# Performance work log

Hardware: AMD Instinct MI355X
Metric: run time of the kernel (lower is better)

The kernel has to match this reference:

```python
import jax, jax.numpy as jnp
import numpy as np

N_E = 1024
E_DIM = 256
BETA = 0.25


def setup_inputs() -> dict:
    key = jax.random.key(0)
    k1, k2 = jax.random.split(key)
    z = jax.random.normal(k1, (16, E_DIM, 64, 64), dtype=jnp.float32)
    # nn.Embedding weight init: uniform(-1/n_e, 1/n_e)
    embedding = jax.random.uniform(
        k2, (N_E, E_DIM), dtype=jnp.float32, minval=-1.0 / N_E, maxval=1.0 / N_E
    )
    return {"z": z, "embedding": embedding}


def reference(z, embedding):
    n_e, e_dim = embedding.shape
    # 'b c ... -> b ... c'
    zt = jnp.moveaxis(z, 1, -1)  # [B, H, W, C]
    zf = zt.reshape(-1, e_dim)   # [N, C]
    # squared distances ||zf||^2 + ||e||^2 - 2 zf e^T  -> [N, n_e]
    d = (
        jnp.sum(zf * zf, axis=1, keepdims=True)
        + jnp.sum(embedding * embedding, axis=1)
        - 2.0 * (zf @ embedding.T)
    )
    idx = jnp.argmin(d, axis=1)  # [N] int32
    # direct embedding gather (equivalent to one-hot @ embedding)
    z_q = embedding[idx].reshape(zt.shape)  # [B, H, W, C]
    # commitment / codebook loss (reduction='mean')
    loss = jnp.mean((jax.lax.stop_gradient(z_q) - zt) ** 2) + BETA * jnp.mean(
        (z_q - jax.lax.stop_gradient(zt)) ** 2
    )
    # straight-through estimator
    z_q_st = zt + jax.lax.stop_gradient(z_q - zt)
    # perplexity from code usage histogram (equals mean of one-hot rows)
    counts = jnp.zeros((n_e,), dtype=jnp.float32).at[idx].add(1.0)
    e_mean = counts / zf.shape[0]
    perplexity = jnp.exp(-jnp.sum(e_mean * jnp.log(e_mean + 1e-10)))
    # 'b ... c -> b c ...'
    z_q_out = jnp.moveaxis(z_q_st, -1, 1)  # [B, C, H, W]
    return z_q_out, loss, perplexity, idx
```

## Files before the change

### kernel.cpp

```cpp
#include <hip/hip_runtime.h>

typedef _Float16 half8 __attribute__((ext_vector_type(8)));
typedef float f32x16 __attribute__((ext_vector_type(16)));

#define EDIM 256
#define NE   1024
#define HW   4096

#define ZQ_OFF   0
#define LOSS_OFF 16777216
#define PERP_OFF 16777217
#define IDX_OFF  16777218

#define WS_ESPH    0
#define WS_BNORM   (1024*1024)
#define WS_COUNTS  (WS_BNORM + 4096)
#define WS_COUNTER (WS_COUNTS + 4096)
#define WS_LOSS    (WS_COUNTER + 16)
#define WS_AN      (WS_LOSS + 16)
#define WS_IDX     (WS_AN + 65536*4)
#define WS_LIST    (WS_IDX + 65536*4)
#define WS_ET      (WS_LIST + 65536*4)

#define EPS 3.0e-4f
#define GEPS (512.0f * EPS)

#define AS1 __attribute__((address_space(1)))
#define AS3 __attribute__((address_space(3)))

__device__ __forceinline__ float np_half128(const float* __restrict__ p, long stride) {
#pragma clang fp contract(off)
    float r[8];
#pragma unroll
    for (int j = 0; j < 8; ++j) { float v = p[(long)j * stride]; r[j] = v * v; }
    for (int i = 8; i < 128; i += 8) {
#pragma unroll
        for (int j = 0; j < 8; ++j) { float v = p[(long)(i + j) * stride]; r[j] += v * v; }
    }
    return ((r[0] + r[1]) + (r[2] + r[3])) + ((r[4] + r[5]) + (r[6] + r[7]));
}

__global__ void k_prep_e(const float* __restrict__ e, _Float16* __restrict__ eh) {
    int t = blockIdx.x * 256 + threadIdx.x;
    int j = t >> 8, c = t & 255;
    float v = e[t] * 1024.0f;
    _Float16 h = (_Float16)v;
    int jt = j >> 7, nt = (j >> 5) & 3, lm = j & 31;
    int kc = c >> 5, r = c & 31, kh = r >> 4, hb = (r >> 3) & 1, kk = r & 7;
    int chunk = (((jt * 8 + kc) * 4 + nt) * 2 + kh) * 64 + hb * 32 + lm;
    eh[chunk * 8 + kk] = h;
}

__global__ void k_transpose(const float* __restrict__ e, float* __restrict__ eT) {
    __shared__ float tile[32][257];
    int b = blockIdx.x;
    int t = threadIdx.x;
#pragma unroll
    for (int i = 0; i < 32; ++i)
        tile[i][t] = e[(size_t)(32 * b + i) * 256 + t];
    __syncthreads();
    int jl = t & 31, cg = t >> 5;
#pragma unroll
    for (int k = 0; k < 32; ++k) {
        int c = cg * 32 + k;
        eT[(size_t)c * 1024 + 32 * b + jl] = tile[jl][c];
    }
}

__global__ void k_bnorm(const float* __restrict__ e, float* __restrict__ Bn) {
    int j = blockIdx.x * 256 + threadIdx.x;
    const float* p = e + (size_t)j * EDIM;
    Bn[j] = np_half128(p, 1) + np_half128(p + 128, 1);
}

__global__ __launch_bounds__(512, 2) void k_dist(
    const float* __restrict__ z, const _Float16* __restrict__ eh,
    const float* __restrict__ Bn, int* __restrict__ idxw,
    float* __restrict__ out, int* __restrict__ counter, int* __restrict__ list,
    double* __restrict__ loss_sum, int* __restrict__ counts,
    float* __restrict__ An)
{
    __shared__ uint4  sB[2][4096];
    __shared__ double lsum[16];
    __shared__ int    lflag[256];
    __shared__ int    lcnt;
    __shared__ int    lbase;

    const int t  = threadIdx.x;
    const int w  = t >> 6;
    const int L  = t & 63;
    const int l5 = L & 31;
    const int hb = L >> 5;
    const int n0 = blockIdx.x * 256;
    const int b  = n0 >> 12, hw0 = n0 & 4095;
    const float* zb = z + (size_t)b * (EDIM * HW) + hw0;
    const int rbase = w * 32;

    if (t == 0) lcnt = 0;

    const uint4* gB4 = (const uint4*)eh;
    const int wb = t & 448;

#pragma unroll
    for (int i = 0; i < 8; ++i)
        __builtin_amdgcn_global_load_lds(
            (const AS1 void*)(gB4 + (i * 512 + t)),
            (AS3 void*)(&sB[0][i * 512 + wb]), 16, 0, 0);

    half8 Ah[16];
    double aSred;
    {
        int m = rbase + l5;
        float r[8]; float A1 = 0.f, Aval;
#pragma unroll
        for (int ks = 0; ks < 16; ++ks) {
            float av[8], pv[8];
#pragma unroll
            for (int j = 0; j < 8; ++j)
                av[j] = zb[(ks * 16 + hb * 8 + j) * HW + m];
#pragma unroll
            for (int j = 0; j < 8; ++j)
                pv[j] = __shfl_xor(av[j], 32, 64);
            {
#pragma clang fp contract(off)
#pragma unroll
                for (int j = 0; j < 8; ++j) {
                    float a0 = hb ? pv[j] : av[j];
                    float a1 = hb ? av[j] : pv[j];
                    if ((ks & 7) == 0) r[j] = a0 * a0;
                    else               r[j] += a0 * a0;
                    r[j] += a1 * a1;
                }
            }
#pragma unroll
            for (int j = 0; j < 8; ++j)
                Ah[ks][j] = (_Float16)av[j];
            if (ks == 7) {
#pragma clang fp contract(off)
                A1 = ((r[0] + r[1]) + (r[2] + r[3])) + ((r[4] + r[5]) + (r[6] + r[7]));
            }
        }
        {
#pragma clang fp contract(off)
            float A2 = ((r[0] + r[1]) + (r[2] + r[3])) + ((r[4] + r[5]) + (r[6] + r[7]));
            Aval = A1 + A2;
        }
        if (hb == 0) An[n0 + m] = Aval;
        double aS = (hb == 0) ? (double)Aval : 0.0;
#pragma unroll
        for (int s = 1; s < 32; s <<= 1) aS += __shfl_xor(aS, s, 64);
        aSred = aS;
    }

    f32x16 acc[4];
#pragma unroll
    for (int nt = 0; nt < 4; ++nt)
#pragma unroll
        for (int r = 0; r < 16; ++r) acc[nt][r] = 0.f;

    float g1[16], g2[16]; int i1[16];
#pragma unroll
    for (int r = 0; r < 16; ++r) { g1[r] = -1e30f; g2[r] = -1e30f; i1[r] = 0; }

    __syncthreads();

    for (int jt = 0; jt < 8; ++jt) {
        const int buf = jt & 1;
        if (jt < 7) {
#pragma unroll
            for (int i = 0; i < 8; ++i)
                __builtin_amdgcn_global_load_lds(
                    (const AS1 void*)(gB4 + ((jt + 1) * 4096 + i * 512 + t)),
                    (AS3 void*)(&sB[buf ^ 1][i * 512 + wb]), 16, 0, 0);
        }

#pragma unroll
        for (int kc = 0; kc < 8; ++kc) {
#pragma unroll
            for (int kh = 0; kh < 2; ++kh) {
#pragma unroll
                for (int nt = 0; nt < 4; ++nt) {
                    half8 bh = *(const half8*)&sB[buf][((kc * 4 + nt) * 2 + kh) * 64 + L];
                    acc[nt] = __builtin_amdgcn_mfma_f32_32x32x16_f16(
                        Ah[kc * 2 + kh], bh, acc[nt], 0, 0, 0);
                }
            }
        }

        float en512[4];
#pragma unroll
        for (int nt = 0; nt < 4; ++nt)
            en512[nt] = 512.0f * Bn[jt * 128 + nt * 32 + l5];
#pragma unroll
        for (int nt = 0; nt < 4; ++nt) {
            int jc = jt * 128 + nt * 32 + l5;
#pragma unroll
            for (int r = 0; r < 16; ++r) {
                float v = acc[nt][r] - en512[nt];
                g2[r] = fmaxf(g2[r], fminf(v, g1[r]));
                bool gt = v > g1[r];
                g1[r] = fmaxf(v, g1[r]);
                i1[r] = gt ? jc : i1[r];
                acc[nt][r] = 0.f;
            }
        }

        __syncthreads();
    }

    double lossP = 0.0;
#pragma unroll
    for (int r = 0; r < 16; ++r) {
        float v1 = g1[r], v2 = g2[r]; int ii = i1[r];
#pragma unroll
        for (int s = 1; s < 32; s <<= 1) {
            float o1 = __shfl_xor(v1, s, 64);
            int   oi = __shfl_xor(ii, s, 64);
            float o2 = __shfl_xor(v2, s, 64);
            float lo = fminf(v1, o1);
            if (o1 > v1 || (o1 == v1 && oi < ii)) { v1 = o1; ii = oi; }
            v2 = fmaxf(fmaxf(v2, o2), lo);
        }
        if (l5 == 0) {
            int rloc = rbase + 4 * hb + (r & 3) + 8 * (r >> 2);
            int n = n0 + rloc;
            idxw[n] = ii;
            out[IDX_OFF + n] = (float)ii;
            atomicAdd(&counts[ii], 1);
            lossP += -(double)v1 * (1.0 / 512.0);
            if (v1 - v2 < GEPS) {
                int p = atomicAdd(&lcnt, 1);
                if (p < 256) lflag[p] = n;
            }
        }
    }
    if (l5 == 0) lsum[w * 2 + hb] = lossP + aSred;
    __syncthreads();
    if (t == 0) {
        double s = 0.0;
#pragma unroll
        for (int i = 0; i < 16; ++i) s += lsum[i];
        atomicAdd(loss_sum, s);
        lbase = lcnt ? atomicAdd(counter, lcnt) : 0;
    }
    __syncthreads();
    for (int i = t; i < lcnt; i += 512) {
        int p = lbase + i;
        if (p < 65536) list[p] = lflag[i];
    }
}

__global__ __launch_bounds__(256, 2) void k_refine(
    const float* __restrict__ z, const float* __restrict__ eT,
    const float* __restrict__ Bn, const float* __restrict__ An,
    const int* __restrict__ counter, const int* __restrict__ list,
    int* __restrict__ idxw, float* __restrict__ out,
    int* __restrict__ counts)
{
    __shared__ float zs[8][256];
    __shared__ int   ns[8];
    __shared__ float ans[8];
    __shared__ float pv[4][8];
    __shared__ int   pi[4][8];
    int t = threadIdx.x;
    int cnt = min(*counter, 65536);
    for (int li0 = blockIdx.x * 8; li0 < cnt; li0 += gridDim.x * 8) {
        int nrows = min(8, cnt - li0);
        __syncthreads();
        if (t < 8) {
            int n = (t < nrows) ? list[li0 + t] : list[li0];
            ns[t] = n; ans[t] = An[n];
        }
        __syncthreads();
#pragma unroll
        for (int u = 0; u < 8; ++u) {
            int n = ns[u];
            zs[u][t] = z[(size_t)(n >> 12) * (EDIM * HW) + (n & 4095) + t * HW];
        }
        __syncthreads();

        float D[4][8];
#pragma unroll
        for (int q = 0; q < 4; ++q)
#pragma unroll
            for (int r = 0; r < 8; ++r) D[q][r] = 0.f;

        for (int c4 = 0; c4 < 64; ++c4) {
            float4 ec[4];
#pragma unroll
            for (int cc = 0; cc < 4; ++cc)
                ec[cc] = *(const float4*)&eT[(size_t)(c4 * 4 + cc) * 1024 + 4 * t];
            float4 zr[8];
#pragma unroll
            for (int r = 0; r < 8; ++r)
                zr[r] = *(const float4*)&zs[r][c4 * 4];
#pragma unroll
            for (int cc = 0; cc < 4; ++cc) {
                const float* ep = (const float*)&ec[cc];
#pragma unroll
                for (int r = 0; r < 8; ++r) {
                    float zv = ((const float*)&zr[r])[cc];
                    D[0][r] = __builtin_fmaf(ep[0], zv, D[0][r]);
                    D[1][r] = __builtin_fmaf(ep[1], zv, D[1][r]);
                    D[2][r] = __builtin_fmaf(ep[2], zv, D[2][r]);
                    D[3][r] = __builtin_fmaf(ep[3], zv, D[3][r]);
                }
            }
        }

        float bm[8]; int bi[8];
#pragma unroll
        for (int r = 0; r < 8; ++r) { bm[r] = 1e30f; bi[r] = 1 << 30; }
        float4 bn4 = *(const float4*)&Bn[4 * t];
        {
#pragma clang fp contract(off)
#pragma unroll
            for (int q = 0; q < 4; ++q) {
                float bnj = ((const float*)&bn4)[q];
                int j = 4 * t + q;
#pragma unroll
                for (int r = 0; r < 8; ++r) {
                    float t2 = D[q][r] + D[q][r];
                    float s  = ans[r] + bnj;
                    float d  = s - t2;
                    if (d < bm[r]) { bm[r] = d; bi[r] = j; }
                }
            }
        }
        int wv = t >> 6, L = t & 63;
#pragma unroll
        for (int r = 0; r < 8; ++r) {
            float v = bm[r]; int ii = bi[r];
#pragma unroll
            for (int s = 1; s < 64; s <<= 1) {
                float ov = __shfl_xor(v, s, 64);
                int   oi = __shfl_xor(ii, s, 64);
                if (ov < v || (ov == v && oi < ii)) { v = ov; ii = oi; }
            }
            if (L == 0) { pv[wv][r] = v; pi[wv][r] = ii; }
        }
        __syncthreads();
        if (t < nrows) {
            float v = pv[0][t]; int ii = pi[0][t];
#pragma unroll
            for (int w2 = 1; w2 < 4; ++w2)
                if (pv[w2][t] < v || (pv[w2][t] == v && pi[w2][t] < ii)) { v = pv[w2][t]; ii = pi[w2][t]; }
            int n = ns[t];
            int old = idxw[n];
            if (old != ii) {
                idxw[n] = ii;
                out[IDX_OFF + n] = (float)ii;
                atomicSub(&counts[old], 1);
                atomicAdd(&counts[ii], 1);
            }
        }
    }
}

__global__ void k_gather(const float* __restrict__ e, const int* __restrict__ idxw,
                         float* __restrict__ out) {
    __shared__ int   jrow[256];
    __shared__ float Ls[8][260];
    int t = threadIdx.x;
    int rg = blockIdx.x >> 1, ch = blockIdx.x & 1;
    int n0 = rg * 256;
    int b = n0 >> 12, hw0 = n0 & 4095;
    jrow[t] = idxw[n0 + t];
    float* zqb = out + ZQ_OFF + (size_t)b * (EDIM * HW) + hw0 + (size_t)ch * 128 * HW;
    int w = t >> 6, L = t & 63;
    __syncthreads();

    for (int cc = 0; cc < 16; ++cc) {
        const float4* ep = (const float4*)(e + (size_t)jrow[t] * EDIM + ch * 128 + cc * 8);
        float4 v0 = ep[0], v1 = ep[1];
        Ls[0][t] = v0.x; Ls[1][t] = v0.y; Ls[2][t] = v0.z; Ls[3][t] = v0.w;
        Ls[4][t] = v1.x; Ls[5][t] = v1.y; Ls[6][t] = v1.z; Ls[7][t] = v1.w;
        __syncthreads();
#pragma unroll
        for (int i = 0; i < 2; ++i) {
            int c = w * 2 + i;
            float4 vv = *(const float4*)&Ls[c][L * 4];
            *(float4*)(zqb + (size_t)(cc * 8 + c) * HW + L * 4) = vv;
        }
        __syncthreads();
    }
}

__global__ void k_final(const int* __restrict__ counts, const double* __restrict__ loss_sum,
                        float* __restrict__ out) {
    __shared__ float sred[4];
    int t = threadIdx.x;
    float s = 0.f;
    for (int qq = 0; qq < 4; ++qq) {
        float p = (float)counts[qq * 256 + t] * (1.0f / 65536.0f);
        s += p * logf(p + 1e-10f);
    }
#pragma unroll
    for (int sh = 1; sh < 64; sh <<= 1) s += __shfl_xor(s, sh, 64);
    if ((t & 63) == 0) sred[t >> 6] = s;
    __syncthreads();
    if (t == 0) {
        out[PERP_OFF] = expf(-(sred[0] + sred[1] + sred[2] + sred[3]));
        out[LOSS_OFF] = (float)(*loss_sum * 1.25 / 16777216.0);
    }
}

extern "C" void kernel_launch(void* const* d_in, const int* in_sizes, int n_in,
                              void* d_out, int out_size, void* d_ws, size_t ws_size,
                              hipStream_t stream) {
    const float* z = (const float*)d_in[0];
    const float* e = (const float*)d_in[1];
    float* out = (float*)d_out;
    char* ws = (char*)d_ws;

    _Float16* eh      = (_Float16*)(ws + WS_ESPH);
    float*    Bn      = (float*)(ws + WS_BNORM);
    int*      counts  = (int*)(ws + WS_COUNTS);
    int*      counter = (int*)(ws + WS_COUNTER);
    double*   loss_sum= (double*)(ws + WS_LOSS);
    float*    An      = (float*)(ws + WS_AN);
    int*      idxw    = (int*)(ws + WS_IDX);
    int*      list    = (int*)(ws + WS_LIST);
    float*    eT      = (float*)(ws + WS_ET);

    hipMemsetAsync(ws + WS_COUNTS, 0, 4096 + 16 + 16, stream);

    k_prep_e   <<<1024, 256, 0, stream>>>(e, eh);
    k_transpose<<<32,   256, 0, stream>>>(e, eT);
    k_bnorm    <<<4,    256, 0, stream>>>(e, Bn);
    k_dist     <<<256,  512, 0, stream>>>(z, eh, Bn, idxw, out, counter, list, loss_sum, counts, An);
    k_refine   <<<2048, 256, 0, stream>>>(z, eT, Bn, An, counter, list, idxw, out, counts);
    k_gather   <<<512,  256, 0, stream>>>(e, idxw, out);
    k_final    <<<1,    256, 0, stream>>>(counts, loss_sum, out);
}
```

Measured before the change: 239.0 us.

## Fuse codebook gather into distance kernel and patch refined rows in refine kernel

The separate gather kernel is removed. Each k_dist block now writes z_q for its own 256 rows from the argmin indices it holds in shared memory, and k_refine rewrites only the rows whose index changed. The codebook norm computation is also folded into the transpose kernel, which drops another launch. This saves two kernel launches and an index round trip through global memory, but it lengthens k_dist's tail and makes refine do scattered strided writes.

```diff
diff --git a/kernel.cpp b/kernel.cpp
--- a/kernel.cpp
+++ b/kernel.cpp
@@ -28,18 +28,6 @@
 #define AS1 __attribute__((address_space(1)))
 #define AS3 __attribute__((address_space(3)))
 
-__device__ __forceinline__ float np_half128(const float* __restrict__ p, long stride) {
-#pragma clang fp contract(off)
-    float r[8];
-#pragma unroll
-    for (int j = 0; j < 8; ++j) { float v = p[(long)j * stride]; r[j] = v * v; }
-    for (int i = 8; i < 128; i += 8) {
-#pragma unroll
-        for (int j = 0; j < 8; ++j) { float v = p[(long)(i + j) * stride]; r[j] += v * v; }
-    }
-    return ((r[0] + r[1]) + (r[2] + r[3])) + ((r[4] + r[5]) + (r[6] + r[7]));
-}
-
 __global__ void k_prep_e(const float* __restrict__ e, _Float16* __restrict__ eh) {
     int t = blockIdx.x * 256 + threadIdx.x;
     int j = t >> 8, c = t & 255;
@@ -51,7 +39,8 @@
     eh[chunk * 8 + kk] = h;
 }
 
-__global__ void k_transpose(const float* __restrict__ e, float* __restrict__ eT) {
+__global__ void k_transpose(const float* __restrict__ e, float* __restrict__ eT,
+                            float* __restrict__ Bn) {
     __shared__ float tile[32][257];
     int b = blockIdx.x;
     int t = threadIdx.x;
@@ -65,24 +54,39 @@
         int c = cg * 32 + k;
         eT[(size_t)c * 1024 + 32 * b + jl] = tile[jl][c];
     }
-}
-
-__global__ void k_bnorm(const float* __restrict__ e, float* __restrict__ Bn) {
-    int j = blockIdx.x * 256 + threadIdx.x;
-    const float* p = e + (size_t)j * EDIM;
-    Bn[j] = np_half128(p, 1) + np_half128(p + 128, 1);
+    int row = t >> 3, q = t & 7;
+    float A[2];
+#pragma unroll
+    for (int h = 0; h < 2; ++h) {
+#pragma clang fp contract(off)
+        float acc = 0.f;
+        for (int i = 0; i < 16; ++i) {
+            float v = tile[row][h * 128 + i * 8 + q];
+            float sq = v * v;
+            acc = (i == 0) ? sq : acc + sq;
+        }
+#pragma unroll
+        for (int s = 1; s < 8; s <<= 1) acc += __shfl_xor(acc, s, 64);
+        A[h] = acc;
+    }
+    if (q == 0) {
+#pragma clang fp contract(off)
+        Bn[32 * b + row] = A[0] + A[1];
+    }
 }
 
 __global__ __launch_bounds__(512, 2) void k_dist(
     const float* __restrict__ z, const _Float16* __restrict__ eh,
-    const float* __restrict__ Bn, int* __restrict__ idxw,
-    float* __restrict__ out, int* __restrict__ counter, int* __restrict__ list,
+    const float* __restrict__ e, const float* __restrict__ Bn,
+    int* __restrict__ idxw, float* __restrict__ out,
+    int* __restrict__ counter, int* __restrict__ list,
     double* __restrict__ loss_sum, int* __restrict__ counts,
     float* __restrict__ An)
 {
     __shared__ uint4  sB[2][4096];
     __shared__ double lsum[16];
     __shared__ int    lflag[256];
+    __shared__ int    idxs[256];
     __shared__ int    lcnt;
     __shared__ int    lbase;
 
@@ -225,6 +229,7 @@
             int rloc = rbase + 4 * hb + (r & 3) + 8 * (r >> 2);
             int n = n0 + rloc;
             idxw[n] = ii;
+            idxs[rloc] = ii;
             out[IDX_OFF + n] = (float)ii;
             atomicAdd(&counts[ii], 1);
             lossP += -(double)v1 * (1.0 / 512.0);
@@ -248,10 +253,41 @@
         int p = lbase + i;
         if (p < 65536) list[p] = lflag[i];
     }
+
+    {
+        float* Ls = (float*)&sB[0][0];
+        const int r_ = t & 255;
+        const int hf = t >> 8;
+        const int jc = idxs[r_];
+        const float* er = e + (size_t)jc * EDIM + hf * 128;
+        float* zqb = out + ZQ_OFF + (size_t)b * (EDIM * HW) + hw0;
+        for (int cc = 0; cc < 16; ++cc) {
+            float4 v0 = *(const float4*)(er + cc * 8);
+            float4 v1 = *(const float4*)(er + cc * 8 + 4);
+            __syncthreads();
+            Ls[(hf * 8 + 0) * 260 + r_] = v0.x;
+            Ls[(hf * 8 + 1) * 260 + r_] = v0.y;
+            Ls[(hf * 8 + 2) * 260 + r_] = v0.z;
+            Ls[(hf * 8 + 3) * 260 + r_] = v0.w;
+            Ls[(hf * 8 + 4) * 260 + r_] = v1.x;
+            Ls[(hf * 8 + 5) * 260 + r_] = v1.y;
+            Ls[(hf * 8 + 6) * 260 + r_] = v1.z;
+            Ls[(hf * 8 + 7) * 260 + r_] = v1.w;
+            __syncthreads();
+#pragma unroll
+            for (int i = 0; i < 2; ++i) {
+                int cslot = w * 2 + i;
+                int c = (cslot >= 8 ? 128 : 0) + cc * 8 + (cslot & 7);
+                float4 vv = *(const float4*)&Ls[cslot * 260 + L * 4];
+                *(float4*)(zqb + (size_t)c * HW + L * 4) = vv;
+            }
+        }
+    }
 }
 
 __global__ __launch_bounds__(256, 2) void k_refine(
     const float* __restrict__ z, const float* __restrict__ eT,
+    const float* __restrict__ e,
     const float* __restrict__ Bn, const float* __restrict__ An,
     const int* __restrict__ counter, const int* __restrict__ list,
     int* __restrict__ idxw, float* __restrict__ out,
@@ -262,6 +298,8 @@
     __shared__ float ans[8];
     __shared__ float pv[4][8];
     __shared__ int   pi[4][8];
+    __shared__ int   chgN[8], chgJ[8];
+    __shared__ int   nchg;
     int t = threadIdx.x;
     int cnt = min(*counter, 65536);
     for (int li0 = blockIdx.x * 8; li0 < cnt; li0 += gridDim.x * 8) {
@@ -271,6 +309,7 @@
             int n = (t < nrows) ? list[li0 + t] : list[li0];
             ns[t] = n; ans[t] = An[n];
         }
+        if (t == 255) nchg = 0;
         __syncthreads();
 #pragma unroll
         for (int u = 0; u < 8; ++u) {
@@ -352,37 +391,16 @@
                 out[IDX_OFF + n] = (float)ii;
                 atomicSub(&counts[old], 1);
                 atomicAdd(&counts[ii], 1);
-            }
-        }
-    }
-}
-
-__global__ void k_gather(const float* __restrict__ e, const int* __restrict__ idxw,
-                         float* __restrict__ out) {
-    __shared__ int   jrow[256];
-    __shared__ float Ls[8][260];
-    int t = threadIdx.x;
-    int rg = blockIdx.x >> 1, ch = blockIdx.x & 1;
-    int n0 = rg * 256;
-    int b = n0 >> 12, hw0 = n0 & 4095;
-    jrow[t] = idxw[n0 + t];
-    float* zqb = out + ZQ_OFF + (size_t)b * (EDIM * HW) + hw0 + (size_t)ch * 128 * HW;
-    int w = t >> 6, L = t & 63;
-    __syncthreads();
-
-    for (int cc = 0; cc < 16; ++cc) {
-        const float4* ep = (const float4*)(e + (size_t)jrow[t] * EDIM + ch * 128 + cc * 8);
-        float4 v0 = ep[0], v1 = ep[1];
-        Ls[0][t] = v0.x; Ls[1][t] = v0.y; Ls[2][t] = v0.z; Ls[3][t] = v0.w;
-        Ls[4][t] = v1.x; Ls[5][t] = v1.y; Ls[6][t] = v1.z; Ls[7][t] = v1.w;
-        __syncthreads();
-#pragma unroll
-        for (int i = 0; i < 2; ++i) {
-            int c = w * 2 + i;
-            float4 vv = *(const float4*)&Ls[c][L * 4];
-            *(float4*)(zqb + (size_t)(cc * 8 + c) * HW + L * 4) = vv;
-        }
-        __syncthreads();
+                int p = atomicAdd(&nchg, 1);
+                chgN[p] = n; chgJ[p] = ii;
+            }
+        }
+        __syncthreads();
+        for (int u = 0; u < nchg; ++u) {
+            int n = chgN[u], jj = chgJ[u];
+            out[ZQ_OFF + (size_t)(n >> 12) * (EDIM * HW) + (size_t)t * HW + (n & 4095)]
+                = e[jj * 256 + t];
+        }
     }
 }
 
@@ -426,10 +444,8 @@
     hipMemsetAsync(ws + WS_COUNTS, 0, 4096 + 16 + 16, stream);
 
     k_prep_e   <<<1024, 256, 0, stream>>>(e, eh);
-    k_transpose<<<32,   256, 0, stream>>>(e, eT);
-    k_bnorm    <<<4,    256, 0, stream>>>(e, Bn);
-    k_dist     <<<256,  512, 0, stream>>>(z, eh, Bn, idxw, out, counter, list, loss_sum, counts, An);
-    k_refine   <<<2048, 256, 0, stream>>>(z, eT, Bn, An, counter, list, idxw, out, counts);
-    k_gather   <<<512,  256, 0, stream>>>(e, idxw, out);
+    k_transpose<<<32,   256, 0, stream>>>(e, eT, Bn);
+    k_dist     <<<256,  512, 0, stream>>>(z, eh, e, Bn, idxw, out, counter, list, loss_sum, counts, An);
+    k_refine   <<<2048, 256, 0, stream>>>(z, eT, e, Bn, An, counter, list, idxw, out, counts);
     k_final    <<<1,    256, 0, stream>>>(counts, loss_sum, out);
 }
```

New measurement: 227.8 us. 1.05x faster.
